# Kernel optimization log

Measured on AMD Instinct MI355X. Metric: run time of the kernel, lower is better.

The kernel has to match this reference:

```python
import jax, jax.numpy as jnp
import numpy as np

D = 256
K = 3  # depthwise conv kernel size (odd)
A_EPS = 1e-4
POW_MIN = 1e-20
LN_EPS = 1e-5


def setup_inputs() -> dict:
    key = jax.random.key(0)
    ks = jax.random.split(key, 10)
    B, H, W = 8, 96, 96
    x = jax.random.normal(ks[0], (B, H, W, D), dtype=jnp.float32)
    inp = {
        'x': x,
        'ln_g': jnp.ones((D,), jnp.float32),
        'ln_b': jnp.zeros((D,), jnp.float32),
        'w_in': jax.random.normal(ks[1], (D, 2 * D), jnp.float32) * 0.02,
        'b_in': jnp.zeros((2 * D,), jnp.float32),
        'conv_w': jax.random.normal(ks[2], (K, K, 1, D), jnp.float32) * 0.1,
        'conv_b': jnp.zeros((D,), jnp.float32),
        'a_logit': 7.0 + 0.1 * jax.random.normal(ks[3], (D,), jnp.float32),
        'ssm_b': jnp.ones((D,), jnp.float32) + 0.02 * jax.random.normal(ks[4], (D,), jnp.float32),
        'ssm_c': jnp.ones((D,), jnp.float32) + 0.02 * jax.random.normal(ks[5], (D,), jnp.float32),
        'ssm_d': jnp.ones((D,), jnp.float32) + 0.02 * jax.random.normal(ks[6], (D,), jnp.float32),
        'w_out': jax.random.normal(ks[7], (D, D), jnp.float32) * 0.02,
        'b_out': jnp.zeros((D,), jnp.float32),
    }
    return inp


def _ssm_scan(x, a_logit, b, c, d):
    # x: (N, L, D). s_t = a*s_{t-1} + b*x_t ; y_t = c*s_t + d*x_t
    # via log-domain cumsum reformulation (as in the torch source).
    L = x.shape[1]
    a = jnp.clip(jax.nn.sigmoid(a_logit), A_EPS, 1.0 - A_EPS)  # (D,)
    t = jnp.arange(L, dtype=jnp.float32)
    a_pow = jnp.maximum(jnp.exp(t[:, None] * jnp.log(a)[None, :]), POW_MIN)  # (L,D)
    u = x * b  # (N,L,D)
    r = jnp.cumsum(u / a_pow[None], axis=1)
    return r * a_pow[None] * c + x * d


def reference(x, ln_g, ln_b, w_in, b_in, conv_w, conv_b,
              a_logit, ssm_b, ssm_c, ssm_d, w_out, b_out):
    B, H, W, Dm = x.shape
    x0 = x
    # LayerNorm over channel dim
    mu = jnp.mean(x, axis=-1, keepdims=True)
    var = jnp.mean(jnp.square(x - mu), axis=-1, keepdims=True)
    h = (x - mu) * jax.lax.rsqrt(var + LN_EPS) * ln_g + ln_b
    # in_proj -> split into value and gate
    xg = h @ w_in + b_in  # (B,H,W,2D)
    x_in, gate = jnp.split(xg, 2, axis=-1)
    gate = jax.nn.sigmoid(gate)
    # depthwise conv (SAME padding) + SiLU, NHWC layout
    u = jax.lax.conv_general_dilated(
        x_in, conv_w, window_strides=(1, 1), padding='SAME',
        dimension_numbers=('NHWC', 'HWIO', 'NHWC'), feature_group_count=Dm)
    u = jax.nn.silu(u + conv_b)
    # 2D bidirectional scan mixing
    L = H * W
    seq_row = u.reshape(B, L, Dm)
    seq_col = u.transpose(0, 2, 1, 3).reshape(B, L, Dm)

    def bid(s):
        yf = _ssm_scan(s, a_logit, ssm_b, ssm_c, ssm_d)
        yb = jnp.flip(_ssm_scan(jnp.flip(s, axis=1), a_logit, ssm_b, ssm_c, ssm_d), axis=1)
        return 0.5 * (yf + yb)

    y_row = bid(seq_row).reshape(B, H, W, Dm)
    y_col = bid(seq_col).reshape(B, W, H, Dm).transpose(0, 2, 1, 3)
    y = 0.5 * (y_row + y_col)
    # gate, out_proj, residual
    y = y * gate
    y = y @ w_out + b_out
    return x0 + y
```

## Files before the change

### kernel.cpp

```cpp
#include <hip/hip_runtime.h>
#include <math.h>

#define DD   256
#define HHH  96
#define WWW  96
#define NB   8
#define LL   9216
#define NPIX (NB*LL)
#define TCH  32
#define NCH  (LL/TCH)

typedef __bf16 bf16_8 __attribute__((ext_vector_type(8)));
typedef float  f32_4  __attribute__((ext_vector_type(4)));

static __device__ __forceinline__ float sigmoidf_(float x) {
    return 1.0f / (1.0f + expf(-x));
}

template<int DIR>
static __device__ __forceinline__ int spidx(int t) {
    if (DIR == 0) return t;
    int w = t / HHH;
    int h = t - w * HHH;
    return h * WWW + w;
}

__global__ __launch_bounds__(256) void wcvt_kernel(const float* __restrict__ w_in,
                                                   const float* __restrict__ w_out,
                                                   __bf16* __restrict__ w_inT,
                                                   __bf16* __restrict__ w_outT) {
    int i = blockIdx.x * 256 + threadIdx.x;
    int n = i >> 8, k = i & 255;
    w_inT[i] = (__bf16)w_in[k * 512 + n];
    if (i < 256 * 256) w_outT[i] = (__bf16)w_out[k * 256 + n];
}

__global__ __launch_bounds__(256) void ln_kernel(const float* __restrict__ x,
                                                 const float* __restrict__ g,
                                                 const float* __restrict__ b,
                                                 __bf16* __restrict__ h) {
    int pix = blockIdx.x;
    int d = threadIdx.x;
    float v = x[(size_t)pix * DD + d];
    float s = v, s2 = v * v;
    #pragma unroll
    for (int o = 32; o > 0; o >>= 1) {
        s  += __shfl_down(s, o, 64);
        s2 += __shfl_down(s2, o, 64);
    }
    __shared__ float ws1[4], ws2[4];
    int wid = d >> 6, lane = d & 63;
    if (lane == 0) { ws1[wid] = s; ws2[wid] = s2; }
    __syncthreads();
    if (d == 0) {
        float a = 0.f, c = 0.f;
        for (int i = 0; i < 4; i++) { a += ws1[i]; c += ws2[i]; }
        ws1[0] = a; ws2[0] = c;
    }
    __syncthreads();
    float mu  = ws1[0] * (1.0f / 256.0f);
    float var = ws2[0] * (1.0f / 256.0f) - mu * mu;
    float r = rsqrtf(var + 1e-5f);
    h[(size_t)pix * DD + d] = (__bf16)((v - mu) * r * g[d] + b[d]);
}

template<int MODE>
__global__ __launch_bounds__(256) void gemm_bf16(const __bf16* __restrict__ A,
                                                 const __bf16* __restrict__ BT,
                                                 const float* __restrict__ bias,
                                                 __bf16* __restrict__ out_xin,
                                                 __bf16* __restrict__ out_gate,
                                                 float* __restrict__ out_f32,
                                                 const float* __restrict__ x0) {
    const int K = 256;
    __shared__ __bf16 As[128 * 40];
    __shared__ __bf16 Bs[128 * 40];
    int tid = threadIdx.x;
    int lane = tid & 63, wv = tid >> 6;
    int rowBase = blockIdx.x * 128;
    int colBase = blockIdx.y * 128;
    int ldr = tid >> 2;
    int seg = tid & 3;

    f32_4 acc[4][4];
    #pragma unroll
    for (int i = 0; i < 4; i++)
        #pragma unroll
        for (int j = 0; j < 4; j++) acc[i][j] = (f32_4){0.f, 0.f, 0.f, 0.f};

    const __bf16* Aip = A + (size_t)(rowBase + ldr) * K + seg * 8;
    const __bf16* Bip = BT + (size_t)(colBase + ldr) * K + seg * 8;
    int m0 = (wv >> 1) * 64, n0 = (wv & 1) * 64;
    int fr = lane & 15, fq = lane >> 4;

    for (int k0 = 0; k0 < K; k0 += 32) {
        uint4 a0 = *(const uint4*)(Aip + k0);
        uint4 a1 = *(const uint4*)(Aip + (size_t)64 * K + k0);
        uint4 b0 = *(const uint4*)(Bip + k0);
        uint4 b1 = *(const uint4*)(Bip + (size_t)64 * K + k0);
        __syncthreads();
        *(uint4*)&As[ldr * 40 + seg * 8]        = a0;
        *(uint4*)&As[(ldr + 64) * 40 + seg * 8] = a1;
        *(uint4*)&Bs[ldr * 40 + seg * 8]        = b0;
        *(uint4*)&Bs[(ldr + 64) * 40 + seg * 8] = b1;
        __syncthreads();
        bf16_8 af[4], bb[4];
        #pragma unroll
        for (int mi = 0; mi < 4; mi++)
            af[mi] = *(const bf16_8*)&As[(m0 + mi * 16 + fr) * 40 + fq * 8];
        #pragma unroll
        for (int ni = 0; ni < 4; ni++)
            bb[ni] = *(const bf16_8*)&Bs[(n0 + ni * 16 + fr) * 40 + fq * 8];
        #pragma unroll
        for (int mi = 0; mi < 4; mi++)
            #pragma unroll
            for (int ni = 0; ni < 4; ni++)
                acc[mi][ni] = __builtin_amdgcn_mfma_f32_16x16x32_bf16(
                    af[mi], bb[ni], acc[mi][ni], 0, 0, 0);
    }

    int rowW = rowBase + m0 + fq * 4;
    int colW = colBase + n0 + fr;
    #pragma unroll
    for (int mi = 0; mi < 4; mi++) {
        #pragma unroll
        for (int ni = 0; ni < 4; ni++) {
            int col = colW + ni * 16;
            float bv = bias[col];
            #pragma unroll
            for (int r = 0; r < 4; r++) {
                int row = rowW + mi * 16 + r;
                float v = acc[mi][ni][r] + bv;
                if (MODE == 0) {
                    if (col < 256) {
                        out_xin[(size_t)row * 256 + col] = (__bf16)v;
                    } else {
                        out_gate[(size_t)row * 256 + (col - 256)] = (__bf16)sigmoidf_(v);
                    }
                } else {
                    out_f32[(size_t)row * 256 + col] = v + x0[(size_t)row * 256 + col];
                }
            }
        }
    }
}

static __device__ __forceinline__ void loadcol(const __bf16* __restrict__ xin,
                                               int b, int h, int w, int d,
                                               float c[3]) {
    if (w < 0 || w >= WWW) { c[0] = c[1] = c[2] = 0.f; return; }
    size_t base = ((size_t)b * LL + (size_t)h * WWW + w) * DD + d;
    c[0] = (h > 0)       ? (float)xin[base - (size_t)WWW * DD] : 0.f;
    c[1] = (float)xin[base];
    c[2] = (h + 1 < HHH) ? (float)xin[base + (size_t)WWW * DD] : 0.f;
}

__global__ __launch_bounds__(256) void conv_tot_kernel(const __bf16* __restrict__ xin,
                                                       const float* __restrict__ cw,
                                                       const float* __restrict__ cb,
                                                       const float* __restrict__ a_logit,
                                                       const float* __restrict__ ssm_b,
                                                       __bf16* __restrict__ u,
                                                       float* __restrict__ tot_f,
                                                       float* __restrict__ tot_b) {
    int cx = blockIdx.x, h = blockIdx.y, b = blockIdx.z;
    int d = threadIdx.x;
    int w0 = cx * TCH;
    float k[9];
    #pragma unroll
    for (int i = 0; i < 9; i++) k[i] = cw[i * DD + d];
    float bias = cb[d];
    float a = sigmoidf_(a_logit[d]);
    a = fminf(fmaxf(a, 1e-4f), 1.0f - 1e-4f);
    float bb = ssm_b[d];

    float cl[3], cc[3], cr[3];
    loadcol(xin, b, h, w0 - 1, d, cl);
    loadcol(xin, b, h, w0,     d, cc);
    loadcol(xin, b, h, w0 + 1, d, cr);

    float v[TCH];
    float sf = 0.f;
    size_t outBase = ((size_t)b * LL + (size_t)h * WWW + w0) * DD + d;
    #pragma unroll
    for (int j = 0; j < TCH; j++) {
        float nx[3];
        loadcol(xin, b, h, w0 + j + 2, d, nx);
        float acc = bias;
        acc += k[0] * cl[0] + k[1] * cc[0] + k[2] * cr[0];
        acc += k[3] * cl[1] + k[4] * cc[1] + k[5] * cr[1];
        acc += k[6] * cl[2] + k[7] * cc[2] + k[8] * cr[2];
        float uv = acc * sigmoidf_(acc);
        v[j] = uv;
        u[outBase + (size_t)j * DD] = (__bf16)uv;
        sf = a * sf + bb * uv;
        cl[0] = cc[0]; cl[1] = cc[1]; cl[2] = cc[2];
        cc[0] = cr[0]; cc[1] = cr[1]; cc[2] = cr[2];
        cr[0] = nx[0]; cr[1] = nx[1]; cr[2] = nx[2];
    }
    int chunk = h * 3 + cx;
    tot_f[((size_t)b * NCH + chunk) * DD + d] = sf;
    float sb = 0.f;
    #pragma unroll
    for (int j = TCH - 1; j >= 0; j--) sb = a * sb + bb * v[j];
    tot_b[((size_t)b * NCH + chunk) * DD + d] = sb;
}

__global__ __launch_bounds__(256) void scan_totals_col(const __bf16* __restrict__ u,
                                                       const float* __restrict__ a_logit,
                                                       const float* __restrict__ ssm_b,
                                                       float* __restrict__ tot_f,
                                                       float* __restrict__ tot_b) {
    int blk = blockIdx.x;
    int b = blk / NCH, c = blk - b * NCH;
    int d = threadIdx.x;
    float a = sigmoidf_(a_logit[d]);
    a = fminf(fmaxf(a, 1e-4f), 1.0f - 1e-4f);
    float bb = ssm_b[d];
    size_t base = (size_t)b * LL * DD;
    int t0 = c * TCH;
    float v[TCH];
    #pragma unroll
    for (int j = 0; j < TCH; j++)
        v[j] = (float)u[base + (size_t)spidx<1>(t0 + j) * DD + d];
    float s = 0.f;
    #pragma unroll
    for (int j = 0; j < TCH; j++) s = a * s + bb * v[j];
    tot_f[(size_t)blk * DD + d] = s;
    s = 0.f;
    #pragma unroll
    for (int j = TCH - 1; j >= 0; j--) s = a * s + bb * v[j];
    tot_b[(size_t)blk * DD + d] = s;
}

__global__ __launch_bounds__(256) void scan_carries(const float* __restrict__ tot_all,
                                                    const float* __restrict__ a_logit,
                                                    float* __restrict__ car_all) {
    int b = blockIdx.x;
    int var = blockIdx.y;
    int d = threadIdx.x;
    float a = sigmoidf_(a_logit[d]);
    a = fminf(fmaxf(a, 1e-4f), 1.0f - 1e-4f);
    float a2 = a * a, a4 = a2 * a2, a8 = a4 * a4, a16 = a8 * a8;
    float q = a16 * a16;
    const float* tot = tot_all + (size_t)var * NB * NCH * DD + (size_t)b * NCH * DD + d;
    float* car = car_all + (size_t)var * NB * NCH * DD + (size_t)b * NCH * DD + d;
    float P = 0.f;
    if ((var & 1) == 0) {
        for (int c0 = 0; c0 < NCH; c0 += 8) {
            float t[8];
            #pragma unroll
            for (int j = 0; j < 8; j++) t[j] = tot[(size_t)(c0 + j) * DD];
            #pragma unroll
            for (int j = 0; j < 8; j++) {
                car[(size_t)(c0 + j) * DD] = P;
                P = q * P + t[j];
            }
        }
    } else {
        for (int c0 = NCH - 8; c0 >= 0; c0 -= 8) {
            float t[8];
            #pragma unroll
            for (int j = 0; j < 8; j++) t[j] = tot[(size_t)(c0 + j) * DD];
            #pragma unroll
            for (int j = 7; j >= 0; j--) {
                car[(size_t)(c0 + j) * DD] = P;
                P = q * P + t[j];
            }
        }
    }
}

template<int DIR>
__global__ __launch_bounds__(256) void scan_apply(const __bf16* __restrict__ u,
                                                  const float* __restrict__ a_logit,
                                                  const float* __restrict__ ssm_b,
                                                  const float* __restrict__ ssm_c,
                                                  const float* __restrict__ ssm_d,
                                                  const float* __restrict__ car_f,
                                                  const float* __restrict__ car_b,
                                                  float* __restrict__ y,
                                                  const __bf16* __restrict__ gate,
                                                  __bf16* __restrict__ g) {
    int blk = blockIdx.x;
    int b = blk / NCH, c = blk - b * NCH;
    int d = threadIdx.x;
    float a = sigmoidf_(a_logit[d]);
    a = fminf(fmaxf(a, 1e-4f), 1.0f - 1e-4f);
    float bb = ssm_b[d], cc = ssm_c[d], dd = ssm_d[d];
    size_t base = (size_t)b * LL * DD;
    int t0 = c * TCH;
    float v[TCH];
    #pragma unroll
    for (int j = 0; j < TCH; j++)
        v[j] = (float)u[base + (size_t)spidx<DIR>(t0 + j) * DD + d];
    float yf[TCH];
    float s = car_f[(size_t)blk * DD + d];
    #pragma unroll
    for (int j = 0; j < TCH; j++) {
        s = a * s + bb * v[j];
        yf[j] = cc * s + dd * v[j];
    }
    s = car_b[(size_t)blk * DD + d];
    #pragma unroll
    for (int j = TCH - 1; j >= 0; j--) {
        s = a * s + bb * v[j];
        float val = 0.25f * (yf[j] + cc * s + dd * v[j]);
        size_t idx = base + (size_t)spidx<DIR>(t0 + j) * DD + d;
        if (DIR == 0) {
            y[idx] = val;
        } else {
            float t = y[idx] + val;
            g[idx] = (__bf16)(t * (float)gate[idx]);
        }
    }
}

extern "C" void kernel_launch(void* const* d_in, const int* in_sizes, int n_in,
                              void* d_out, int out_size, void* d_ws, size_t ws_size,
                              hipStream_t stream) {
    const float* x       = (const float*)d_in[0];
    const float* ln_g    = (const float*)d_in[1];
    const float* ln_b    = (const float*)d_in[2];
    const float* w_in    = (const float*)d_in[3];
    const float* b_in    = (const float*)d_in[4];
    const float* conv_w  = (const float*)d_in[5];
    const float* conv_b  = (const float*)d_in[6];
    const float* a_logit = (const float*)d_in[7];
    const float* ssm_b   = (const float*)d_in[8];
    const float* ssm_c   = (const float*)d_in[9];
    const float* ssm_d   = (const float*)d_in[10];
    const float* w_out   = (const float*)d_in[11];
    const float* b_out   = (const float*)d_in[12];
    float* out = (float*)d_out;

    char* ws = (char*)d_ws;
    const size_t SZH = (size_t)NPIX * DD * sizeof(__bf16);
    const size_t TS  = (size_t)NB * NCH * DD * sizeof(float);

    __bf16* hB     = (__bf16*)(ws);
    __bf16* xinB   = (__bf16*)(ws + SZH);
    __bf16* uB     = (__bf16*)(ws + 2 * SZH);
    __bf16* gateB  = (__bf16*)(ws + 3 * SZH);
    float*  tot    = (float*)(ws + 4 * SZH);
    float*  car    = (float*)(ws + 4 * SZH + 4 * TS);
    __bf16* w_inT  = (__bf16*)(ws + 4 * SZH + 8 * TS);
    __bf16* w_outT = w_inT + 512 * 256;
    float* y = out;

    wcvt_kernel<<<512, 256, 0, stream>>>(w_in, w_out, w_inT, w_outT);
    ln_kernel<<<NPIX, 256, 0, stream>>>(x, ln_g, ln_b, hB);
    gemm_bf16<0><<<dim3(NPIX / 128, 4), 256, 0, stream>>>(hB, w_inT, b_in,
                                                          xinB, gateB, nullptr, nullptr);
    conv_tot_kernel<<<dim3(WWW / TCH, HHH, NB), 256, 0, stream>>>(
        xinB, conv_w, conv_b, a_logit, ssm_b, uB,
        tot + 0 * (size_t)NB * NCH * DD, tot + 1 * (size_t)NB * NCH * DD);
    scan_totals_col<<<NB * NCH, 256, 0, stream>>>(
        uB, a_logit, ssm_b,
        tot + 2 * (size_t)NB * NCH * DD, tot + 3 * (size_t)NB * NCH * DD);
    scan_carries<<<dim3(NB, 4), 256, 0, stream>>>(tot, a_logit, car);
    scan_apply<0><<<NB * NCH, 256, 0, stream>>>(
        uB, a_logit, ssm_b, ssm_c, ssm_d,
        car + 0 * (size_t)NB * NCH * DD, car + 1 * (size_t)NB * NCH * DD,
        y, nullptr, nullptr);
    scan_apply<1><<<NB * NCH, 256, 0, stream>>>(
        uB, a_logit, ssm_b, ssm_c, ssm_d,
        car + 2 * (size_t)NB * NCH * DD, car + 3 * (size_t)NB * NCH * DD,
        y, gateB, hB);
    gemm_bf16<1><<<dim3(NPIX / 128, 2), 256, 0, stream>>>(hB, w_outT, b_out,
                                                          nullptr, nullptr, out, x);
}
```

Measured before the change: 449.2 us.

## Rework GEMM tiling, vectorize LayerNorm, store row-scan intermediate in bf16

The GEMM now keeps the whole 128-column B slab (full K) in LDS, loaded once per block. Each wave streams its own 64 A rows straight from global memory into registers with one-step prefetch, and blocks cover 256 rows. This removes the per-k-step barriers and the A staging through LDS. LayerNorm processes four pixels per block, one wave each, with float4 loads and no shared-memory reduction. The row-direction scan result is stored as bf16 in the free xin buffer instead of fp32 in the output, halving that round-trip traffic but adding rounding error.

```diff
diff --git a/kernel.cpp b/kernel.cpp
--- a/kernel.cpp
+++ b/kernel.cpp
@@ -11,6 +11,7 @@
 #define NCH  (LL/TCH)
 
 typedef __bf16 bf16_8 __attribute__((ext_vector_type(8)));
+typedef __bf16 bf16_4 __attribute__((ext_vector_type(4)));
 typedef float  f32_4  __attribute__((ext_vector_type(4)));
 
 static __device__ __forceinline__ float sigmoidf_(float x) {
@@ -39,92 +40,96 @@
                                                  const float* __restrict__ g,
                                                  const float* __restrict__ b,
                                                  __bf16* __restrict__ h) {
-    int pix = blockIdx.x;
-    int d = threadIdx.x;
-    float v = x[(size_t)pix * DD + d];
-    float s = v, s2 = v * v;
+    int wv = threadIdx.x >> 6, lane = threadIdx.x & 63;
+    int pix = blockIdx.x * 4 + wv;
+    float4 v = *(const float4*)&x[(size_t)pix * DD + lane * 4];
+    float s  = v.x + v.y + v.z + v.w;
+    float s2 = v.x * v.x + v.y * v.y + v.z * v.z + v.w * v.w;
     #pragma unroll
     for (int o = 32; o > 0; o >>= 1) {
-        s  += __shfl_down(s, o, 64);
-        s2 += __shfl_down(s2, o, 64);
-    }
-    __shared__ float ws1[4], ws2[4];
-    int wid = d >> 6, lane = d & 63;
-    if (lane == 0) { ws1[wid] = s; ws2[wid] = s2; }
-    __syncthreads();
-    if (d == 0) {
-        float a = 0.f, c = 0.f;
-        for (int i = 0; i < 4; i++) { a += ws1[i]; c += ws2[i]; }
-        ws1[0] = a; ws2[0] = c;
-    }
-    __syncthreads();
-    float mu  = ws1[0] * (1.0f / 256.0f);
-    float var = ws2[0] * (1.0f / 256.0f) - mu * mu;
+        s  += __shfl_xor(s, o, 64);
+        s2 += __shfl_xor(s2, o, 64);
+    }
+    float mu  = s * (1.0f / 256.0f);
+    float var = s2 * (1.0f / 256.0f) - mu * mu;
     float r = rsqrtf(var + 1e-5f);
-    h[(size_t)pix * DD + d] = (__bf16)((v - mu) * r * g[d] + b[d]);
-}
-
+    float4 gg = *(const float4*)&g[lane * 4];
+    float4 bb = *(const float4*)&b[lane * 4];
+    bf16_4 o;
+    o[0] = (__bf16)((v.x - mu) * r * gg.x + bb.x);
+    o[1] = (__bf16)((v.y - mu) * r * gg.y + bb.y);
+    o[2] = (__bf16)((v.z - mu) * r * gg.z + bb.z);
+    o[3] = (__bf16)((v.w - mu) * r * gg.w + bb.w);
+    *(bf16_4*)&h[(size_t)pix * DD + lane * 4] = o;
+}
+
+#define BPITCH 264
 template<int MODE>
-__global__ __launch_bounds__(256) void gemm_bf16(const __bf16* __restrict__ A,
-                                                 const __bf16* __restrict__ BT,
-                                                 const float* __restrict__ bias,
-                                                 __bf16* __restrict__ out_xin,
-                                                 __bf16* __restrict__ out_gate,
-                                                 float* __restrict__ out_f32,
-                                                 const float* __restrict__ x0) {
+__global__ __launch_bounds__(256, 2) void gemm_bf16(const __bf16* __restrict__ A,
+                                                    const __bf16* __restrict__ BT,
+                                                    const float* __restrict__ bias,
+                                                    __bf16* __restrict__ out_xin,
+                                                    __bf16* __restrict__ out_gate,
+                                                    float* __restrict__ out_f32,
+                                                    const float* __restrict__ x0) {
     const int K = 256;
-    __shared__ __bf16 As[128 * 40];
-    __shared__ __bf16 Bs[128 * 40];
+    __shared__ __bf16 Bs[128 * BPITCH];
     int tid = threadIdx.x;
     int lane = tid & 63, wv = tid >> 6;
-    int rowBase = blockIdx.x * 128;
+    int rowBase = blockIdx.x * 256;
     int colBase = blockIdx.y * 128;
-    int ldr = tid >> 2;
-    int seg = tid & 3;
-
-    f32_4 acc[4][4];
+
+    #pragma unroll
+    for (int it = 0; it < 16; it++) {
+        int f = it * 256 + tid;
+        int col = f >> 5;
+        int seg = f & 31;
+        *(uint4*)&Bs[col * BPITCH + seg * 8] =
+            *(const uint4*)&BT[(size_t)(colBase + col) * K + seg * 8];
+    }
+    __syncthreads();
+
+    int fr = lane & 15, fq = lane >> 4;
+    int row0 = rowBase + wv * 64;
+
+    f32_4 acc[4][8];
     #pragma unroll
     for (int i = 0; i < 4; i++)
         #pragma unroll
-        for (int j = 0; j < 4; j++) acc[i][j] = (f32_4){0.f, 0.f, 0.f, 0.f};
-
-    const __bf16* Aip = A + (size_t)(rowBase + ldr) * K + seg * 8;
-    const __bf16* Bip = BT + (size_t)(colBase + ldr) * K + seg * 8;
-    int m0 = (wv >> 1) * 64, n0 = (wv & 1) * 64;
-    int fr = lane & 15, fq = lane >> 4;
-
-    for (int k0 = 0; k0 < K; k0 += 32) {
-        uint4 a0 = *(const uint4*)(Aip + k0);
-        uint4 a1 = *(const uint4*)(Aip + (size_t)64 * K + k0);
-        uint4 b0 = *(const uint4*)(Bip + k0);
-        uint4 b1 = *(const uint4*)(Bip + (size_t)64 * K + k0);
-        __syncthreads();
-        *(uint4*)&As[ldr * 40 + seg * 8]        = a0;
-        *(uint4*)&As[(ldr + 64) * 40 + seg * 8] = a1;
-        *(uint4*)&Bs[ldr * 40 + seg * 8]        = b0;
-        *(uint4*)&Bs[(ldr + 64) * 40 + seg * 8] = b1;
-        __syncthreads();
-        bf16_8 af[4], bb[4];
+        for (int j = 0; j < 8; j++) acc[i][j] = (f32_4){0.f, 0.f, 0.f, 0.f};
+
+    const __bf16* Ap = A + (size_t)(row0 + fr) * K + fq * 8;
+    bf16_8 af[4], afn[4];
+    #pragma unroll
+    for (int mi = 0; mi < 4; mi++)
+        af[mi] = *(const bf16_8*)(Ap + (size_t)mi * 16 * K);
+
+    for (int ks = 0; ks < 8; ks++) {
+        if (ks < 7) {
+            #pragma unroll
+            for (int mi = 0; mi < 4; mi++)
+                afn[mi] = *(const bf16_8*)(Ap + (size_t)mi * 16 * K + (ks + 1) * 32);
+        }
+        bf16_8 bf[8];
+        #pragma unroll
+        for (int ni = 0; ni < 8; ni++)
+            bf[ni] = *(const bf16_8*)&Bs[(ni * 16 + fr) * BPITCH + ks * 32 + fq * 8];
         #pragma unroll
         for (int mi = 0; mi < 4; mi++)
-            af[mi] = *(const bf16_8*)&As[(m0 + mi * 16 + fr) * 40 + fq * 8];
-        #pragma unroll
-        for (int ni = 0; ni < 4; ni++)
-            bb[ni] = *(const bf16_8*)&Bs[(n0 + ni * 16 + fr) * 40 + fq * 8];
-        #pragma unroll
-        for (int mi = 0; mi < 4; mi++)
-            #pragma unroll
-            for (int ni = 0; ni < 4; ni++)
+            #pragma unroll
+            for (int ni = 0; ni < 8; ni++)
                 acc[mi][ni] = __builtin_amdgcn_mfma_f32_16x16x32_bf16(
-                    af[mi], bb[ni], acc[mi][ni], 0, 0, 0);
-    }
-
-    int rowW = rowBase + m0 + fq * 4;
-    int colW = colBase + n0 + fr;
+                    af[mi], bf[ni], acc[mi][ni], 0, 0, 0);
+        #pragma unroll
+        for (int mi = 0; mi < 4; mi++) af[mi] = afn[mi];
+    }
+
+    int rowW = row0 + fq * 4;
+    int colW = colBase + fr;
     #pragma unroll
     for (int mi = 0; mi < 4; mi++) {
         #pragma unroll
-        for (int ni = 0; ni < 4; ni++) {
+        for (int ni = 0; ni < 8; ni++) {
             int col = colW + ni * 16;
             float bv = bias[col];
             #pragma unroll
@@ -279,7 +284,7 @@
                                                   const float* __restrict__ ssm_d,
                                                   const float* __restrict__ car_f,
                                                   const float* __restrict__ car_b,
-                                                  float* __restrict__ y,
+                                                  __bf16* __restrict__ y,
                                                   const __bf16* __restrict__ gate,
                                                   __bf16* __restrict__ g) {
     int blk = blockIdx.x;
@@ -308,9 +313,9 @@
         float val = 0.25f * (yf[j] + cc * s + dd * v[j]);
         size_t idx = base + (size_t)spidx<DIR>(t0 + j) * DD + d;
         if (DIR == 0) {
-            y[idx] = val;
+            y[idx] = (__bf16)val;
         } else {
-            float t = y[idx] + val;
+            float t = (float)y[idx] + val;
             g[idx] = (__bf16)(t * (float)gate[idx]);
         }
     }
@@ -346,11 +351,11 @@
     float*  car    = (float*)(ws + 4 * SZH + 4 * TS);
     __bf16* w_inT  = (__bf16*)(ws + 4 * SZH + 8 * TS);
     __bf16* w_outT = w_inT + 512 * 256;
-    float* y = out;
+    __bf16* yB     = xinB;
 
     wcvt_kernel<<<512, 256, 0, stream>>>(w_in, w_out, w_inT, w_outT);
-    ln_kernel<<<NPIX, 256, 0, stream>>>(x, ln_g, ln_b, hB);
-    gemm_bf16<0><<<dim3(NPIX / 128, 4), 256, 0, stream>>>(hB, w_inT, b_in,
+    ln_kernel<<<NPIX / 4, 256, 0, stream>>>(x, ln_g, ln_b, hB);
+    gemm_bf16<0><<<dim3(NPIX / 256, 4), 256, 0, stream>>>(hB, w_inT, b_in,
                                                           xinB, gateB, nullptr, nullptr);
     conv_tot_kernel<<<dim3(WWW / TCH, HHH, NB), 256, 0, stream>>>(
         xinB, conv_w, conv_b, a_logit, ssm_b, uB,
@@ -362,11 +367,11 @@
     scan_apply<0><<<NB * NCH, 256, 0, stream>>>(
         uB, a_logit, ssm_b, ssm_c, ssm_d,
         car + 0 * (size_t)NB * NCH * DD, car + 1 * (size_t)NB * NCH * DD,
-        y, nullptr, nullptr);
+        yB, nullptr, nullptr);
     scan_apply<1><<<NB * NCH, 256, 0, stream>>>(
         uB, a_logit, ssm_b, ssm_c, ssm_d,
         car + 2 * (size_t)NB * NCH * DD, car + 3 * (size_t)NB * NCH * DD,
-        y, gateB, hB);
-    gemm_bf16<1><<<dim3(NPIX / 128, 2), 256, 0, stream>>>(hB, w_outT, b_out,
+        yB, gateB, hB);
+    gemm_bf16<1><<<dim3(NPIX / 256, 2), 256, 0, stream>>>(hB, w_outT, b_out,
                                                           nullptr, nullptr, out, x);
 }
```

After: 470.8 us. 1.05x slower.
